# Kernel optimization log

Measured on AMD Instinct MI355X. Metric: run time of the kernel, lower is better.

Reference implementation:

```python
import jax, jax.numpy as jnp
import numpy as np

B, L, D = 32, 256, 1024
EPS = 1e-5


def _layernorm(x, w, b):
    m = jnp.mean(x, axis=-1, keepdims=True)
    v = jnp.var(x, axis=-1, keepdims=True)
    return (x - m) * jax.lax.rsqrt(v + EPS) * w + b


def _bitlinear(x, w):
    # BitNet b1.58: ternary weights (per-tensor mean-|w| scale),
    # int8 per-token activations; STE so round() passes gradient through.
    ws = jnp.mean(jnp.abs(w)) + EPS
    wq = jnp.clip(jnp.round(w / ws), -1.0, 1.0) * ws
    wq = w + jax.lax.stop_gradient(wq - w)
    xs = 127.0 / jnp.clip(jnp.max(jnp.abs(x), axis=-1, keepdims=True), EPS, None)
    xq = jnp.clip(jnp.round(x * xs), -128.0, 127.0) / xs
    xq = x + jax.lax.stop_gradient(xq - x)
    return jnp.einsum('bld,od->blo', xq, wq)


def setup_inputs() -> dict:
    key = jax.random.key(0)
    kx, kg, k1, k2 = jax.random.split(key, 4)
    i = np.arange(L)
    # deterministic SHA-256-style rotation wiring
    idx_s0 = np.stack([(i + 7) % L, (i + 18) % L, (i + 3) % L], axis=1)
    idx_s1 = np.stack([(i + 17) % L, (i + 19) % L, (i + 10) % L], axis=1)
    idx_v = np.stack([(i + 32 * j) % L for j in range(1, 9)], axis=1)
    return {
        'x': jax.random.normal(kx, (B, L, D), jnp.float32),
        'ln1_w': jnp.ones((D,), jnp.float32),
        'ln1_b': jnp.zeros((D,), jnp.float32),
        'ln2_w': jnp.ones((D,), jnp.float32),
        'ln2_b': jnp.zeros((D,), jnp.float32),
        'Wg': jax.random.normal(kg, (D, 15 * D), jnp.float32) * 0.02,
        'W1': jax.random.normal(k1, (4 * D, D), jnp.float32) * 0.02,
        'W2': jax.random.normal(k2, (D, 4 * D), jnp.float32) * 0.02,
        'idx_s0': jnp.asarray(idx_s0, jnp.int32),
        'idx_s1': jnp.asarray(idx_s1, jnp.int32),
        'idx_v': jnp.asarray(idx_v, jnp.int32),
    }


def reference(x, ln1_w, ln1_b, ln2_w, ln2_b, Wg, W1, W2, idx_s0, idx_s1, idx_v):
    b = x.shape[0]
    xn = _layernorm(x, ln1_w, ln1_b)  # [B,L,D]

    def gather(idx):  # idx: [L,k] -> [B,L,k*D]
        g = jnp.take(xn, idx.reshape(-1), axis=1)  # [B,L*k,D]
        return g.reshape(b, idx.shape[0], -1)

    combined = jnp.concatenate(
        [xn, gather(idx_s0), gather(idx_s1), gather(idx_v)], axis=-1)  # [B,L,15D]
    x = x + _bitlinear(combined, Wg)
    h = _layernorm(x, ln2_w, ln2_b)
    h = _bitlinear(jax.nn.gelu(_bitlinear(h, W1), approximate=False), W2)
    return x + h
```

## Files before the change

kernel.cpp:

```cpp
#include <hip/hip_runtime.h>
#include <hip/hip_bf16.h>
#include <math.h>
#include <stdint.h>

#define EPS 1e-5f

typedef int v4i __attribute__((ext_vector_type(4)));

__device__ __forceinline__ void glds16(const void* g, void* l) {
  __builtin_amdgcn_global_load_lds(
      (const __attribute__((address_space(1))) void*)g,
      (__attribute__((address_space(3))) void*)l, 16, 0, 0);
}

__device__ __forceinline__ signed char q8(float f, float xs) {
  float r = rintf(f * xs);
  r = fminf(fmaxf(r, -128.f), 127.f);
  return (signed char)(int)r;
}

__device__ __forceinline__ float bf2f(unsigned short h) {
  return __builtin_bit_cast(float, (unsigned)h << 16);
}

__global__ __launch_bounds__(256) void absum3_kernel(const float* __restrict__ Wg,
                                                     const float* __restrict__ W1,
                                                     const float* __restrict__ W2,
                                                     float* __restrict__ out) {
  int blk = blockIdx.x;
  const float* w; long n4; float* o; long lb; long nb;
  if (blk < 512)      { w = Wg; n4 = 3932160; o = &out[0]; lb = blk;       nb = 512; }
  else if (blk < 768) { w = W1; n4 = 1048576; o = &out[1]; lb = blk - 512; nb = 256; }
  else                { w = W2; n4 = 1048576; o = &out[2]; lb = blk - 768; nb = 256; }
  const float4* w4 = (const float4*)w;
  float s = 0.f;
  for (long i = lb * 256 + threadIdx.x; i < n4; i += nb * 256) {
    float4 v = w4[i];
    s += fabsf(v.x) + fabsf(v.y) + fabsf(v.z) + fabsf(v.w);
  }
  for (int off = 32; off; off >>= 1) s += __shfl_down(s, off);
  __shared__ float sb[4];
  int lane = threadIdx.x & 63, wid = threadIdx.x >> 6;
  if (lane == 0) sb[wid] = s;
  __syncthreads();
  if (threadIdx.x == 0) atomicAdd(o, sb[0] + sb[1] + sb[2] + sb[3]);
}

__global__ __launch_bounds__(256) void ternarize3_kernel(const float* __restrict__ Wg,
                                                         const float* __restrict__ W1,
                                                         const float* __restrict__ W2,
                                                         signed char* __restrict__ tg,
                                                         signed char* __restrict__ t1,
                                                         signed char* __restrict__ t2,
                                                         const float* __restrict__ sums) {
  int blk = blockIdx.x;
  const float* w; signed char* t; long n4; float ws; long lb; long nb;
  if (blk < 1024) {
    w = Wg; t = tg; n4 = 3932160; ws = sums[0] * (1.f / 15728640.f) + EPS; lb = blk; nb = 1024;
  } else if (blk < 1536) {
    w = W1; t = t1; n4 = 1048576; ws = sums[1] * (1.f / 4194304.f) + EPS; lb = blk - 1024; nb = 512;
  } else {
    w = W2; t = t2; n4 = 1048576; ws = sums[2] * (1.f / 4194304.f) + EPS; lb = blk - 1536; nb = 512;
  }
  const float4* w4 = (const float4*)w;
  char4* t4 = (char4*)t;
  for (long i = lb * 256 + threadIdx.x; i < n4; i += nb * 256) {
    float4 v = w4[i];
    char4 c;
    c.x = (signed char)(int)fminf(fmaxf(rintf(v.x / ws), -1.f), 1.f);
    c.y = (signed char)(int)fminf(fmaxf(rintf(v.y / ws), -1.f), 1.f);
    c.z = (signed char)(int)fminf(fmaxf(rintf(v.z / ws), -1.f), 1.f);
    c.w = (signed char)(int)fminf(fmaxf(rintf(v.w / ws), -1.f), 1.f);
    t4[i] = c;
  }
}

__global__ __launch_bounds__(256) void ln_rowmax_kernel(const float* __restrict__ x,
                                                        const float* __restrict__ w,
                                                        const float* __restrict__ b,
                                                        float* __restrict__ xn,
                                                        float* __restrict__ rowmax) {
  int m = blockIdx.x;
  int tid = threadIdx.x, lane = tid & 63, wid = tid >> 6;
  __shared__ float sb[4];
  float4 v = ((const float4*)(x + (long)m * 1024))[tid];
  float s = v.x + v.y + v.z + v.w;
  for (int off = 32; off; off >>= 1) s += __shfl_down(s, off);
  if (lane == 0) sb[wid] = s;
  __syncthreads();
  float mean = (sb[0] + sb[1] + sb[2] + sb[3]) * (1.f / 1024.f);
  __syncthreads();
  float dx = v.x - mean, dy = v.y - mean, dz = v.z - mean, dw = v.w - mean;
  float ss = dx * dx + dy * dy + dz * dz + dw * dw;
  for (int off = 32; off; off >>= 1) ss += __shfl_down(ss, off);
  if (lane == 0) sb[wid] = ss;
  __syncthreads();
  float rstd = rsqrtf((sb[0] + sb[1] + sb[2] + sb[3]) * (1.f / 1024.f) + EPS);
  __syncthreads();
  float4 wv = ((const float4*)w)[tid];
  float4 bv = ((const float4*)b)[tid];
  float4 o;
  o.x = dx * rstd * wv.x + bv.x;
  o.y = dy * rstd * wv.y + bv.y;
  o.z = dz * rstd * wv.z + bv.z;
  o.w = dw * rstd * wv.w + bv.w;
  ((float4*)(xn + (long)m * 1024))[tid] = o;
  float mx = fmaxf(fmaxf(fabsf(o.x), fabsf(o.y)), fmaxf(fabsf(o.z), fabsf(o.w)));
  for (int off = 32; off; off >>= 1) mx = fmaxf(mx, __shfl_down(mx, off));
  if (lane == 0) sb[wid] = mx;
  __syncthreads();
  if (tid == 0) rowmax[m] = fmaxf(fmaxf(sb[0], sb[1]), fmaxf(sb[2], sb[3]));
}

__global__ __launch_bounds__(256) void quantA_kernel(const float* __restrict__ xn,
                                                     const int* __restrict__ is0,
                                                     const int* __restrict__ is1,
                                                     const int* __restrict__ iv,
                                                     const float* __restrict__ rowmax,
                                                     const float* __restrict__ sums,
                                                     signed char* __restrict__ Aq,
                                                     float* __restrict__ s1) {
  int m = blockIdx.x;
  int b = m >> 8, l = m & 255;
  const float* rm = rowmax + b * 256;
  int src[15];
  src[0] = l;
#pragma unroll
  for (int j = 0; j < 3; ++j) { src[1 + j] = is0[l * 3 + j]; src[4 + j] = is1[l * 3 + j]; }
#pragma unroll
  for (int j = 0; j < 8; ++j) src[7 + j] = iv[l * 8 + j];
  float c = EPS;
#pragma unroll
  for (int sl = 0; sl < 15; ++sl) c = fmaxf(c, rm[src[sl]]);
  float xs = 127.f / c;
  if (threadIdx.x == 0) s1[m] = (sums[0] * (1.f / 15728640.f) + EPS) * c * (1.f / 127.f);
#pragma unroll
  for (int sl = 0; sl < 15; ++sl) {
    float4 v = ((const float4*)(xn + ((long)(b << 8) + src[sl]) * 1024))[threadIdx.x];
    char4 cc;
    cc.x = q8(v.x, xs); cc.y = q8(v.y, xs); cc.z = q8(v.z, xs); cc.w = q8(v.w, xs);
    *(char4*)&Aq[(long)m * 15360 + sl * 1024 + threadIdx.x * 4] = cc;
  }
}

__global__ __launch_bounds__(256) void ln_quant_acc_kernel(const int* __restrict__ accA,
                                                           const int* accB,
                                                           const float* __restrict__ x,
                                                           const float* __restrict__ s1,
                                                           const float* __restrict__ w,
                                                           const float* __restrict__ bb,
                                                           float* xag,
                                                           signed char* __restrict__ q,
                                                           float* __restrict__ srow,
                                                           const float* __restrict__ sum_ptr,
                                                           float inv_n) {
  int m = blockIdx.x;
  int tid = threadIdx.x, lane = tid & 63, wid = tid >> 6;
  __shared__ float sb[4];
  float sm = s1[m];
  int4 a0 = ((const int4*)(accA + (long)m * 1024))[tid];
  int4 a1 = ((const int4*)(accB + (long)m * 1024))[tid];
  float4 xv = ((const float4*)(x + (long)m * 1024))[tid];
  float4 v;
  v.x = xv.x + sm * (float)(a0.x + a1.x);
  v.y = xv.y + sm * (float)(a0.y + a1.y);
  v.z = xv.z + sm * (float)(a0.z + a1.z);
  v.w = xv.w + sm * (float)(a0.w + a1.w);
  ((float4*)(xag + (long)m * 1024))[tid] = v;
  float s = v.x + v.y + v.z + v.w;
  for (int off = 32; off; off >>= 1) s += __shfl_down(s, off);
  if (lane == 0) sb[wid] = s;
  __syncthreads();
  float mean = (sb[0] + sb[1] + sb[2] + sb[3]) * (1.f / 1024.f);
  __syncthreads();
  float dx = v.x - mean, dy = v.y - mean, dz = v.z - mean, dw = v.w - mean;
  float ss = dx * dx + dy * dy + dz * dz + dw * dw;
  for (int off = 32; off; off >>= 1) ss += __shfl_down(ss, off);
  if (lane == 0) sb[wid] = ss;
  __syncthreads();
  float rstd = rsqrtf((sb[0] + sb[1] + sb[2] + sb[3]) * (1.f / 1024.f) + EPS);
  __syncthreads();
  float4 wv = ((const float4*)w)[tid];
  float4 bv = ((const float4*)bb)[tid];
  float nx = dx * rstd * wv.x + bv.x;
  float ny = dy * rstd * wv.y + bv.y;
  float nz = dz * rstd * wv.z + bv.z;
  float nw = dw * rstd * wv.w + bv.w;
  float mx = fmaxf(fmaxf(fabsf(nx), fabsf(ny)), fmaxf(fabsf(nz), fabsf(nw)));
  for (int off = 32; off; off >>= 1) mx = fmaxf(mx, __shfl_down(mx, off));
  if (lane == 0) sb[wid] = mx;
  __syncthreads();
  float rmax = fmaxf(fmaxf(fmaxf(sb[0], sb[1]), fmaxf(sb[2], sb[3])), EPS);
  float xs = 127.f / rmax;
  char4 c;
  c.x = q8(nx, xs); c.y = q8(ny, xs); c.z = q8(nz, xs); c.w = q8(nw, xs);
  *(char4*)&q[(long)m * 1024 + tid * 4] = c;
  if (tid == 0) srow[m] = (sum_ptr[0] * inv_n + EPS) * rmax * (1.f / 127.f);
}

__global__ __launch_bounds__(256) void rowquant4k_kernel(const unsigned short* __restrict__ g,
                                                         signed char* __restrict__ q,
                                                         float* __restrict__ srow,
                                                         const float* __restrict__ sum_ptr,
                                                         float inv_n) {
  int m = blockIdx.x;
  int tid = threadIdx.x, lane = tid & 63, wid = tid >> 6;
  __shared__ float sb[4];
  const uint4* gr = (const uint4*)(g + (long)m * 4096);
  float f[16];
  float mx = 0.f;
#pragma unroll
  for (int i = 0; i < 2; ++i) {
    uint4 u = gr[tid + i * 256];
    unsigned uu[4] = {u.x, u.y, u.z, u.w};
#pragma unroll
    for (int j = 0; j < 4; ++j) {
      float lo = bf2f((unsigned short)(uu[j] & 0xFFFF));
      float hi = bf2f((unsigned short)(uu[j] >> 16));
      f[i * 8 + j * 2] = lo;
      f[i * 8 + j * 2 + 1] = hi;
      mx = fmaxf(mx, fmaxf(fabsf(lo), fabsf(hi)));
    }
  }
  for (int off = 32; off; off >>= 1) mx = fmaxf(mx, __shfl_down(mx, off));
  if (lane == 0) sb[wid] = mx;
  __syncthreads();
  float rmax = fmaxf(fmaxf(fmaxf(sb[0], sb[1]), fmaxf(sb[2], sb[3])), EPS);
  float xs = 127.f / rmax;
#pragma unroll
  for (int i = 0; i < 2; ++i) {
    char4 c0, c1;
    c0.x = q8(f[i * 8 + 0], xs); c0.y = q8(f[i * 8 + 1], xs);
    c0.z = q8(f[i * 8 + 2], xs); c0.w = q8(f[i * 8 + 3], xs);
    c1.x = q8(f[i * 8 + 4], xs); c1.y = q8(f[i * 8 + 5], xs);
    c1.z = q8(f[i * 8 + 6], xs); c1.w = q8(f[i * 8 + 7], xs);
    long base = (long)m * 4096 + (tid + i * 256) * 8;
    *(char4*)&q[base] = c0;
    *(char4*)&q[base + 4] = c1;
  }
  if (tid == 0) srow[m] = (sum_ptr[0] * inv_n + EPS) * rmax * (1.f / 127.f);
}

__global__ __launch_bounds__(256) void reduce3_kernel(const int* __restrict__ accA,
                                                      const int* __restrict__ accB,
                                                      const float* __restrict__ xag,
                                                      const float* __restrict__ s3,
                                                      float* __restrict__ out) {
  int m = blockIdx.x;
  float sm = s3[m];
  int4 a0 = ((const int4*)(accA + (long)m * 1024))[threadIdx.x];
  int4 a1 = ((const int4*)(accB + (long)m * 1024))[threadIdx.x];
  float4 xv = ((const float4*)(xag + (long)m * 1024))[threadIdx.x];
  float4 o;
  o.x = xv.x + sm * (float)(a0.x + a1.x);
  o.y = xv.y + sm * (float)(a0.y + a1.y);
  o.z = xv.z + sm * (float)(a0.z + a1.z);
  o.w = xv.w + sm * (float)(a0.w + a1.w);
  ((float4*)(out + (long)m * 1024))[threadIdx.x] = o;
}

__global__ __launch_bounds__(256, 4) void gemm_i8(const signed char* __restrict__ A,
                                                  const signed char* __restrict__ Bw,
                                                  __hip_bfloat16* __restrict__ outh,
                                                  int* __restrict__ iacc0,
                                                  int* __restrict__ iacc1,
                                                  const float* __restrict__ scale,
                                                  int N, int K, int kIters, int mode) {
  __shared__ __align__(16) signed char As[128 * 128];
  __shared__ __align__(16) signed char Bs[128 * 128];
  const int tid = threadIdx.x;
  const int lane = tid & 63, wave = tid >> 6;
  const int wm = wave & 1, wn = wave >> 1;
  const long m0 = (long)blockIdx.x * 128;
  const long n0 = (long)blockIdx.y * 128;
  const signed char* Abase = A + m0 * K;
  const signed char* Bbase = Bw + n0 * K;

  v4i acc[4][4] = {};

  const int r15 = lane & 15;
  const int quad = lane >> 4;
  const int sw = lane & 7;

  for (int kt = 0; kt < kIters; ++kt) {
    const long k0 = ((long)blockIdx.z * kIters + kt) << 7;
#pragma unroll
    for (int i = 0; i < 4; ++i) {
      int cb = wave * 64 + i * 256;
      int c = cb + lane;
      long row = c >> 3;
      int blk = (c & 7) ^ ((c >> 3) & 7);
      long colb = (long)blk << 4;
      glds16(Abase + row * K + k0 + colb, &As[cb * 16]);
      glds16(Bbase + row * K + k0 + colb, &Bs[cb * 16]);
    }
    __syncthreads();
#pragma unroll
    for (int ks = 0; ks < 2; ++ks) {
      const int blkb = (ks << 2) + quad;
      const int coff = (blkb ^ sw) << 4;
      v4i af[4], bf[4];
#pragma unroll
      for (int mi = 0; mi < 4; ++mi)
        af[mi] = *(const v4i*)&As[(wm * 64 + mi * 16 + r15) * 128 + coff];
#pragma unroll
      for (int ni = 0; ni < 4; ++ni)
        bf[ni] = *(const v4i*)&Bs[(wn * 64 + ni * 16 + r15) * 128 + coff];
#pragma unroll
      for (int mi = 0; mi < 4; ++mi)
#pragma unroll
        for (int ni = 0; ni < 4; ++ni)
          acc[mi][ni] = __builtin_amdgcn_mfma_i32_16x16x64_i8(af[mi], bf[ni], acc[mi][ni], 0, 0, 0);
    }
    __syncthreads();
  }

  int* iacc = blockIdx.z ? iacc1 : iacc0;
#pragma unroll
  for (int mi = 0; mi < 4; ++mi) {
#pragma unroll
    for (int r = 0; r < 4; ++r) {
      long m = m0 + wm * 64 + mi * 16 + (lane >> 4) * 4 + r;
      if (mode == 2) {
        int* arow = iacc + m * N;
#pragma unroll
        for (int ni = 0; ni < 4; ++ni) {
          long n = n0 + wn * 64 + ni * 16 + (lane & 15);
          arow[n] = acc[mi][ni][r];
        }
      } else {
        float sm = scale[m];
        __hip_bfloat16* orow = outh + m * N;
#pragma unroll
        for (int ni = 0; ni < 4; ++ni) {
          long n = n0 + wn * 64 + ni * 16 + (lane & 15);
          float v = sm * (float)acc[mi][ni][r];
          orow[n] = __float2bfloat16(0.5f * v * (1.f + erff(v * 0.70710678118654752f)));
        }
      }
    }
  }
}

extern "C" void kernel_launch(void* const* d_in, const int* in_sizes, int n_in,
                              void* d_out, int out_size, void* d_ws, size_t ws_size,
                              hipStream_t stream) {
  const float* x    = (const float*)d_in[0];
  const float* ln1w = (const float*)d_in[1];
  const float* ln1b = (const float*)d_in[2];
  const float* ln2w = (const float*)d_in[3];
  const float* ln2b = (const float*)d_in[4];
  const float* Wg   = (const float*)d_in[5];
  const float* W1   = (const float*)d_in[6];
  const float* W2   = (const float*)d_in[7];
  const int* is0    = (const int*)d_in[8];
  const int* is1    = (const int*)d_in[9];
  const int* iv     = (const int*)d_in[10];
  float* out = (float*)d_out;

  char* ws = (char*)d_ws;
  float* sums = (float*)ws;
  signed char* t_g = (signed char*)(ws + 256);
  signed char* t_1 = t_g + 15728640;
  signed char* t_2 = t_1 + 4194304;
  float* rowmax1 = (float*)(t_2 + 4194304);
  float* s1  = rowmax1 + 8192;
  float* s2  = s1 + 8192;
  float* s3  = s2 + 8192;
  float* xag = s3 + 8192;
  int* acc1b = (int*)xag;
  signed char* hq = (signed char*)(xag + 8388608);
  float* xn = (float*)(hq + 8388608);
  int* acc1a = (int*)xn;
  signed char* q3 = (signed char*)xn;
  signed char* Aq = (signed char*)(xn + 8388608);
  unsigned short* gg = (unsigned short*)Aq;
  int* acc3a = (int*)Aq;
  int* acc3b = acc3a + 8192l * 1024;

  hipMemsetAsync(sums, 0, 64, stream);
  absum3_kernel<<<1024, 256, 0, stream>>>(Wg, W1, W2, sums);
  ternarize3_kernel<<<2048, 256, 0, stream>>>(Wg, W1, W2, t_g, t_1, t_2, sums);
  ln_rowmax_kernel<<<8192, 256, 0, stream>>>(x, ln1w, ln1b, xn, rowmax1);
  quantA_kernel<<<8192, 256, 0, stream>>>(xn, is0, is1, iv, rowmax1, sums, Aq, s1);
  gemm_i8<<<dim3(64, 8, 2), 256, 0, stream>>>(Aq, t_g, nullptr, acc1a, acc1b, nullptr,
                                              1024, 15360, 60, 2);
  ln_quant_acc_kernel<<<8192, 256, 0, stream>>>(acc1a, acc1b, x, s1, ln2w, ln2b, xag, hq, s2,
                                                &sums[1], 1.f / 4194304.f);
  gemm_i8<<<dim3(64, 32, 1), 256, 0, stream>>>(hq, t_1, (__hip_bfloat16*)gg, nullptr, nullptr,
                                               s2, 4096, 1024, 8, 1);
  rowquant4k_kernel<<<8192, 256, 0, stream>>>(gg, q3, s3, &sums[2], 1.f / 4194304.f);
  gemm_i8<<<dim3(64, 8, 2), 256, 0, stream>>>(q3, t_2, nullptr, acc3a, acc3b, nullptr,
                                              1024, 4096, 16, 2);
  reduce3_kernel<<<8192, 256, 0, stream>>>(acc3a, acc3b, xag, s3, out);
}
```

Before: 560.4 us.

## Replace int8 GEMM with 8-wave 256x256 double-buffered kernel and XCD-aware tile mapping

The int8 MFMA GEMM moves from 4-wave 128x128 tiles to 8-wave 256x256 tiles. It double-buffers LDS, prefetching k-tile t+2 while computing on t, and uses explicit vmcnt waits, barriers and s_setprio around the MFMA bursts. Block indices are remapped so consecutive tiles land on the same XCD, which is meant to improve L2 reuse. The goals are higher arithmetic intensity per LDS load and hiding global-load latency, at the cost of 128KB LDS per block, large register pressure from a 32-tile accumulator, and fewer blocks (256) for the split-K GEMMs.

Result: slower. 660.2 us (+17.8%).

```diff
diff --git a/kernel.cpp b/kernel.cpp
--- a/kernel.cpp
+++ b/kernel.cpp
@@ -259,83 +259,132 @@
   ((float4*)(out + (long)m * 1024))[threadIdx.x] = o;
 }
 
-__global__ __launch_bounds__(256, 4) void gemm_i8(const signed char* __restrict__ A,
-                                                  const signed char* __restrict__ Bw,
-                                                  __hip_bfloat16* __restrict__ outh,
-                                                  int* __restrict__ iacc0,
-                                                  int* __restrict__ iacc1,
-                                                  const float* __restrict__ scale,
-                                                  int N, int K, int kIters, int mode) {
-  __shared__ __align__(16) signed char As[128 * 128];
-  __shared__ __align__(16) signed char Bs[128 * 128];
+__device__ __forceinline__ void stage8(const signed char* __restrict__ Abase,
+                                       const signed char* __restrict__ Bbase,
+                                       long K, long k0,
+                                       signed char* AsD, signed char* BsD, int tid) {
+  const int w = tid >> 6, lane = tid & 63;
+#pragma unroll
+  for (int i = 0; i < 4; ++i) {
+    int cb = w * 64 + i * 512;
+    int c = cb + lane;
+    long row = c >> 3;
+    int blk = (c & 7) ^ ((c >> 3) & 7);
+    long gcol = k0 + ((long)blk << 4);
+    glds16(Abase + row * K + gcol, AsD + cb * 16);
+    glds16(Bbase + row * K + gcol, BsD + cb * 16);
+  }
+}
+
+__global__ __launch_bounds__(512, 2) void gemm_i8_8w(const signed char* __restrict__ A,
+                                                     const signed char* __restrict__ Bw,
+                                                     __hip_bfloat16* __restrict__ outh,
+                                                     int* __restrict__ iacc0,
+                                                     int* __restrict__ iacc1,
+                                                     const float* __restrict__ scale,
+                                                     int N, long K, int nt, int mode,
+                                                     int nM, int nN) {
+  __shared__ __align__(16) signed char As[2 * 32768];
+  __shared__ __align__(16) signed char Bs[2 * 32768];
   const int tid = threadIdx.x;
-  const int lane = tid & 63, wave = tid >> 6;
-  const int wm = wave & 1, wn = wave >> 1;
-  const long m0 = (long)blockIdx.x * 128;
-  const long n0 = (long)blockIdx.y * 128;
+  const int lane = tid & 63;
+  const int wave = tid >> 6;
+  const int wm = wave >> 2, wn = wave & 3;
+  const int r15 = lane & 15, quad = lane >> 4, sw = lane & 7;
+
+  const int total = (int)gridDim.x;
+  const int b = (int)blockIdx.x;
+  const int g = (b & 7) * (total >> 3) + (b >> 3);
+  const int mt = g % nM;
+  const int rest = g / nM;
+  const int ntl = rest % nN;
+  const int z = rest / nN;
+  const long m0 = (long)mt * 256, n0 = (long)ntl * 256;
   const signed char* Abase = A + m0 * K;
   const signed char* Bbase = Bw + n0 * K;
-
-  v4i acc[4][4] = {};
-
-  const int r15 = lane & 15;
-  const int quad = lane >> 4;
-  const int sw = lane & 7;
-
-  for (int kt = 0; kt < kIters; ++kt) {
-    const long k0 = ((long)blockIdx.z * kIters + kt) << 7;
-#pragma unroll
-    for (int i = 0; i < 4; ++i) {
-      int cb = wave * 64 + i * 256;
-      int c = cb + lane;
-      long row = c >> 3;
-      int blk = (c & 7) ^ ((c >> 3) & 7);
-      long colb = (long)blk << 4;
-      glds16(Abase + row * K + k0 + colb, &As[cb * 16]);
-      glds16(Bbase + row * K + k0 + colb, &Bs[cb * 16]);
+  const long k0base = (long)z * nt * 128;
+
+  v4i acc[8][4] = {};
+
+  stage8(Abase, Bbase, K, k0base, As, Bs, tid);
+  stage8(Abase, Bbase, K, k0base + 128, As + 32768, Bs + 32768, tid);
+  asm volatile("s_waitcnt vmcnt(8)" ::: "memory");
+  __builtin_amdgcn_s_barrier();
+
+  for (int t = 0; t < nt; ++t) {
+    const signed char* Ap = As + (t & 1) * 32768;
+    const signed char* Bp = Bs + (t & 1) * 32768;
+#pragma unroll
+    for (int qm = 0; qm < 2; ++qm) {
+#pragma unroll
+      for (int qn = 0; qn < 2; ++qn) {
+        v4i af[4][2], bfr[2][2];
+#pragma unroll
+        for (int m2 = 0; m2 < 4; ++m2) {
+          const signed char* rp = Ap + (wm * 128 + (qm * 4 + m2) * 16 + r15) * 128;
+          af[m2][0] = *(const v4i*)(rp + ((quad ^ sw) << 4));
+          af[m2][1] = *(const v4i*)(rp + (((quad + 4) ^ sw) << 4));
+        }
+#pragma unroll
+        for (int n2 = 0; n2 < 2; ++n2) {
+          const signed char* rp = Bp + (wn * 64 + (qn * 2 + n2) * 16 + r15) * 128;
+          bfr[n2][0] = *(const v4i*)(rp + ((quad ^ sw) << 4));
+          bfr[n2][1] = *(const v4i*)(rp + (((quad + 4) ^ sw) << 4));
+        }
+        __builtin_amdgcn_s_barrier();
+        __builtin_amdgcn_s_setprio(1);
+#pragma unroll
+        for (int m2 = 0; m2 < 4; ++m2) {
+#pragma unroll
+          for (int n2 = 0; n2 < 2; ++n2) {
+            acc[qm * 4 + m2][qn * 2 + n2] = __builtin_amdgcn_mfma_i32_16x16x64_i8(
+                af[m2][0], bfr[n2][0], acc[qm * 4 + m2][qn * 2 + n2], 0, 0, 0);
+            acc[qm * 4 + m2][qn * 2 + n2] = __builtin_amdgcn_mfma_i32_16x16x64_i8(
+                af[m2][1], bfr[n2][1], acc[qm * 4 + m2][qn * 2 + n2], 0, 0, 0);
+          }
+        }
+        __builtin_amdgcn_s_setprio(0);
+        __builtin_amdgcn_s_barrier();
+      }
     }
-    __syncthreads();
-#pragma unroll
-    for (int ks = 0; ks < 2; ++ks) {
-      const int blkb = (ks << 2) + quad;
-      const int coff = (blkb ^ sw) << 4;
-      v4i af[4], bf[4];
-#pragma unroll
-      for (int mi = 0; mi < 4; ++mi)
-        af[mi] = *(const v4i*)&As[(wm * 64 + mi * 16 + r15) * 128 + coff];
-#pragma unroll
-      for (int ni = 0; ni < 4; ++ni)
-        bf[ni] = *(const v4i*)&Bs[(wn * 64 + ni * 16 + r15) * 128 + coff];
-#pragma unroll
-      for (int mi = 0; mi < 4; ++mi)
+    if (t + 2 < nt) {
+      long k0 = k0base + (long)(t + 2) * 128;
+      stage8(Abase, Bbase, K, k0, As + (t & 1) * 32768, Bs + (t & 1) * 32768, tid);
+      asm volatile("s_waitcnt vmcnt(8)" ::: "memory");
+      __builtin_amdgcn_s_barrier();
+    } else if (t + 1 < nt) {
+      asm volatile("s_waitcnt vmcnt(0)" ::: "memory");
+      __builtin_amdgcn_s_barrier();
+    }
+    __builtin_amdgcn_sched_barrier(0);
+  }
+
+  if (mode == 2) {
+    int* iacc = z ? iacc1 : iacc0;
+#pragma unroll
+    for (int mi = 0; mi < 8; ++mi) {
+#pragma unroll
+      for (int r = 0; r < 4; ++r) {
+        long m = m0 + wm * 128 + mi * 16 + quad * 4 + r;
+        int* arow = iacc + m * N;
 #pragma unroll
         for (int ni = 0; ni < 4; ++ni)
-          acc[mi][ni] = __builtin_amdgcn_mfma_i32_16x16x64_i8(af[mi], bf[ni], acc[mi][ni], 0, 0, 0);
+          arow[n0 + wn * 64 + ni * 16 + r15] = acc[mi][ni][r];
+      }
     }
-    __syncthreads();
-  }
-
-  int* iacc = blockIdx.z ? iacc1 : iacc0;
-#pragma unroll
-  for (int mi = 0; mi < 4; ++mi) {
-#pragma unroll
-    for (int r = 0; r < 4; ++r) {
-      long m = m0 + wm * 64 + mi * 16 + (lane >> 4) * 4 + r;
-      if (mode == 2) {
-        int* arow = iacc + m * N;
-#pragma unroll
-        for (int ni = 0; ni < 4; ++ni) {
-          long n = n0 + wn * 64 + ni * 16 + (lane & 15);
-          arow[n] = acc[mi][ni][r];
-        }
-      } else {
+  } else {
+#pragma unroll
+    for (int mi = 0; mi < 8; ++mi) {
+#pragma unroll
+      for (int r = 0; r < 4; ++r) {
+        long m = m0 + wm * 128 + mi * 16 + quad * 4 + r;
         float sm = scale[m];
         __hip_bfloat16* orow = outh + m * N;
 #pragma unroll
         for (int ni = 0; ni < 4; ++ni) {
-          long n = n0 + wn * 64 + ni * 16 + (lane & 15);
           float v = sm * (float)acc[mi][ni][r];
-          orow[n] = __float2bfloat16(0.5f * v * (1.f + erff(v * 0.70710678118654752f)));
+          orow[n0 + wn * 64 + ni * 16 + r15] =
+              __float2bfloat16(0.5f * v * (1.f + erff(v * 0.70710678118654752f)));
         }
       }
     }
@@ -383,14 +432,14 @@
   ternarize3_kernel<<<2048, 256, 0, stream>>>(Wg, W1, W2, t_g, t_1, t_2, sums);
   ln_rowmax_kernel<<<8192, 256, 0, stream>>>(x, ln1w, ln1b, xn, rowmax1);
   quantA_kernel<<<8192, 256, 0, stream>>>(xn, is0, is1, iv, rowmax1, sums, Aq, s1);
-  gemm_i8<<<dim3(64, 8, 2), 256, 0, stream>>>(Aq, t_g, nullptr, acc1a, acc1b, nullptr,
-                                              1024, 15360, 60, 2);
+  gemm_i8_8w<<<256, 512, 0, stream>>>(Aq, t_g, nullptr, acc1a, acc1b, nullptr,
+                                      1024, 15360L, 60, 2, 32, 4);
   ln_quant_acc_kernel<<<8192, 256, 0, stream>>>(acc1a, acc1b, x, s1, ln2w, ln2b, xag, hq, s2,
                                                 &sums[1], 1.f / 4194304.f);
-  gemm_i8<<<dim3(64, 32, 1), 256, 0, stream>>>(hq, t_1, (__hip_bfloat16*)gg, nullptr, nullptr,
-                                               s2, 4096, 1024, 8, 1);
+  gemm_i8_8w<<<512, 512, 0, stream>>>(hq, t_1, (__hip_bfloat16*)gg, nullptr, nullptr,
+                                      s2, 4096, 1024L, 8, 1, 32, 16);
   rowquant4k_kernel<<<8192, 256, 0, stream>>>(gg, q3, s3, &sums[2], 1.f / 4194304.f);
-  gemm_i8<<<dim3(64, 8, 2), 256, 0, stream>>>(q3, t_2, nullptr, acc3a, acc3b, nullptr,
-                                              1024, 4096, 16, 2);
+  gemm_i8_8w<<<256, 512, 0, stream>>>(q3, t_2, nullptr, acc3a, acc3b, nullptr,
+                                      1024, 4096L, 16, 2, 32, 4);
   reduce3_kernel<<<8192, 256, 0, stream>>>(acc3a, acc3b, xag, s3, out);
 }
```
